# Kernel optimization log

Hardware: AMD Instinct MI355X
Metric: run time of the kernel (lower is better)

Reference implementation:

```python
import jax, jax.numpy as jnp
import numpy as np
from jax import lax

PALETTE = 256


def setup_inputs() -> dict:
    key = jax.random.key(0)
    k1, k2, k3, k4 = jax.random.split(key, 4)
    x = jax.random.normal(k1, (16, 64, 256, 256), dtype=jnp.float32)
    lookup_table = jax.random.normal(k2, (PALETTE,), dtype=jnp.float32) * 0.05
    weight_idx = jax.random.randint(k3, (64, 64, 3, 3), 0, PALETTE, dtype=jnp.int32)
    bias = jax.random.normal(k4, (64,), dtype=jnp.float32) * 0.01
    return {"x": x, "lookup_table": lookup_table, "weight_idx": weight_idx, "bias": bias}


def reference(x, lookup_table, weight_idx, bias):
    # Dequantize: palette gather produces full OIHW weight tensor.
    full_w = lookup_table[weight_idx]  # [O, I, kH, kW] float32
    # conv2d with stride=1, padding=0 (hardcoded in module), dilation=1, groups=1
    out = lax.conv_general_dilated(
        x, full_w,
        window_strides=(1, 1),
        padding='VALID',
        rhs_dilation=(1, 1),
        dimension_numbers=('NCHW', 'OIHW', 'NCHW'),
        feature_group_count=1,
    )
    return out + bias[None, :, None, None]
```

## Files before the change

kernel.cpp:

```cpp
#include <hip/hip_runtime.h>


typedef __bf16 bf16x8 __attribute__((ext_vector_type(8)));
typedef float f32x4 __attribute__((ext_vector_type(4)));
typedef float f32x2 __attribute__((ext_vector_type(2)));

union Frag {
    uint4 q;
    bf16x8 v;
};

__global__ __launch_bounds__(256) void dequant_B(
        const float* __restrict__ lut, const int* __restrict__ widx,
        uint4* __restrict__ Bws) {
    int s = blockIdx.x * 256 + threadIdx.x;
    int l = s & 63;
    int nt = (s >> 6) & 3;
    int kc = s >> 8;
    if (kc >= 18) return;
    int r = kc >> 1;
    int kh = r / 3, kw = r - kh * 3;
    int o = nt * 16 + (l & 15);
    int c0 = (kc & 1) * 32 + (l >> 4) * 8;
    Frag f;
#pragma unroll
    for (int j = 0; j < 8; ++j) {
        int c = c0 + j;
        int idx = widx[((o * 64 + c) * 3 + kh) * 3 + kw];
        f.v[j] = (__bf16)lut[idx];
    }
    Bws[s] = f.q;
}

#define A_CB 530

__global__ __launch_bounds__(256, 4) void conv_mfma(
        const float* __restrict__ x, const float* __restrict__ bias,
        const uint4* __restrict__ Bws, float* __restrict__ out) {
    __shared__ uint4 ldsA[4 * A_CB];
    unsigned* lds32 = (unsigned*)ldsA;

    int bx = blockIdx.x;
    int owt = bx & 1;
    int rem = bx >> 1;
    int ohp = rem % 127;
    int n   = rem / 127;
    int ow0 = owt * 128;
    int oh0 = ohp * 2;
    int t = threadIdx.x;

    const float* xn = x + (size_t)n * (64 * 256 * 256);

    int w = t >> 6;
    int l = t & 63;
    int l15 = l & 15, l4 = l >> 4;

    int tl_cb  = t & 3;
    int tl_rc  = t >> 2;
    int tl_rr  = tl_rc >> 1;
    int tl_col = 128 + (tl_rc & 1);
    int tl_xc  = ow0 + tl_col; if (tl_xc > 255) tl_xc = 255;

    int ohl = w >> 1;
    int ob  = (w & 1) * 2;

    f32x4 acc[8][2] = {};

    for (int h = 0; h < 2; ++h) {
        {
            const float* cbase = xn + (size_t)(((h * 4 + w) * 8 + l4 * 2)) * 65536
                                 + ow0;
#pragma unroll
            for (int ch2 = 0; ch2 < 2; ++ch2) {
                const float* pb = cbase + ch2 * 64 + l15 * 4;
                f32x4 f0[4], f1[4];
#pragma unroll
                for (int rr = 0; rr < 4; ++rr) {
                    const float* p = pb + (oh0 + rr) * 256;
                    f0[rr] = *(const f32x4*)(p);
                    f1[rr] = *(const f32x4*)(p + 65536);
                }
#pragma unroll
                for (int rr = 0; rr < 4; ++rr) {
                    int gbase = w * A_CB + rr * 132 + ch2 * 64 + l15 * 4;
#pragma unroll
                    for (int i = 0; i < 4; ++i) {
                        union { __bf16 hh[2]; unsigned u; } bp;
                        bp.hh[0] = (__bf16)f0[rr][i];
                        bp.hh[1] = (__bf16)f1[rr][i];
                        lds32[(gbase + i) * 4 + l4] = bp.u;
                    }
                }
            }
            if (t < 32) {
                const float* src = xn + (size_t)((h * 4 + tl_cb) * 8) * 65536
                                   + (oh0 + tl_rr) * 256 + tl_xc;
                Frag f;
#pragma unroll
                for (int j = 0; j < 8; ++j)
                    f.v[j] = (__bf16)src[j * 65536];
                ldsA[tl_cb * A_CB + tl_rr * 132 + tl_col] = f.q;
            }
        }
        __syncthreads();

#pragma unroll
        for (int i = 0; i < 9; ++i) {
            int kh = i / 3, kw = i - kh * 3;
            int kc = 2 * i + h;

            Frag b[2];
#pragma unroll
            for (int nt = 0; nt < 2; ++nt)
                b[nt].q = Bws[(kc * 4 + ob + nt) * 64 + l];

            Frag a[8];
#pragma unroll
            for (int mt = 0; mt < 8; ++mt)
                a[mt].q = ldsA[l4 * A_CB + (ohl + kh) * 132 + l15 + kw + mt * 16];

#pragma unroll
            for (int mt = 0; mt < 8; ++mt)
#pragma unroll
                for (int nt = 0; nt < 2; ++nt)
                    acc[mt][nt] = __builtin_amdgcn_mfma_f32_16x16x32_bf16(
                        a[mt].v, b[nt].v, acc[mt][nt], 0, 0, 0);
        }
        __syncthreads();
    }

    float* slab = (float*)ldsA + w * (16 * 130);
    int oseg = (w & 1) * 32;
    int oh = oh0 + ohl;
    float* orow = out + ((size_t)n * 64 * 254 + oh) * 254 + ow0;
    bool ok = (ow0 + l * 2 + 1) < 254;
#pragma unroll
    for (int nt = 0; nt < 2; ++nt) {
#pragma unroll
        for (int mt = 0; mt < 8; ++mt)
#pragma unroll
            for (int rg = 0; rg < 4; ++rg)
                slab[l15 * 130 + mt * 16 + l4 * 4 + rg] = acc[mt][nt][rg];
#pragma unroll
        for (int j = 0; j < 16; ++j) {
            int o = oseg + nt * 16 + j;
            float bv = bias[o];
            f32x2 v;
            v[0] = slab[j * 130 + l * 2]     + bv;
            v[1] = slab[j * 130 + l * 2 + 1] + bv;
            if (ok)
                *(f32x2*)(orow + (size_t)o * (254 * 254) + l * 2) = v;
        }
    }
}

extern "C" void kernel_launch(void* const* d_in, const int* in_sizes, int n_in,
                              void* d_out, int out_size, void* d_ws, size_t ws_size,
                              hipStream_t stream) {
    const float* x    = (const float*)d_in[0];
    const float* lut  = (const float*)d_in[1];
    const int*   widx = (const int*)d_in[2];
    const float* bias = (const float*)d_in[3];
    float* out = (float*)d_out;
    uint4* Bws = (uint4*)d_ws;

    dequant_B<<<18, 256, 0, stream>>>(lut, widx, Bws);
    conv_mfma<<<16 * 127 * 2, 256, 0, stream>>>(x, bias, (const uint4*)Bws, out);
}
```

Before: 490.9 us.

## Process full output row width per block with 512 threads to share halo

Each block now computes two full 254-wide output rows using 8 waves instead of two 128-wide halves with 4 waves. This removes the separate halo-column staging path and the redundant reloads of overlapping input columns across blocks. In exchange the block uses roughly twice the LDS, which limits how many blocks fit per CU, and the epilogue slab stride changes to 129.

```diff
diff --git a/kernel.cpp b/kernel.cpp
--- a/kernel.cpp
+++ b/kernel.cpp
@@ -32,20 +32,18 @@
     Bws[s] = f.q;
 }
 
-#define A_CB 530
+#define A_ROW 258
+#define A_CBL 1034
 
-__global__ __launch_bounds__(256, 4) void conv_mfma(
+__global__ __launch_bounds__(512, 4) void conv_mfma(
         const float* __restrict__ x, const float* __restrict__ bias,
         const uint4* __restrict__ Bws, float* __restrict__ out) {
-    __shared__ uint4 ldsA[4 * A_CB];
+    __shared__ uint4 ldsA[4136];
     unsigned* lds32 = (unsigned*)ldsA;
 
     int bx = blockIdx.x;
-    int owt = bx & 1;
-    int rem = bx >> 1;
-    int ohp = rem % 127;
-    int n   = rem / 127;
-    int ow0 = owt * 128;
+    int ohp = bx % 127;
+    int n   = bx / 127;
     int oh0 = ohp * 2;
     int t = threadIdx.x;
 
@@ -55,51 +53,39 @@
     int l = t & 63;
     int l15 = l & 15, l4 = l >> 4;
 
-    int tl_cb  = t & 3;
-    int tl_rc  = t >> 2;
-    int tl_rr  = tl_rc >> 1;
-    int tl_col = 128 + (tl_rc & 1);
-    int tl_xc  = ow0 + tl_col; if (tl_xc > 255) tl_xc = 255;
-
-    int ohl = w >> 1;
-    int ob  = (w & 1) * 2;
+    int st_cbl = w & 3;
+    int st_rp  = w >> 2;
+    int ohl = (w >> 2) & 1;
+    int owh = (w >> 1) & 1;
+    int og  = w & 1;
 
     f32x4 acc[8][2] = {};
 
     for (int h = 0; h < 2; ++h) {
         {
-            const float* cbase = xn + (size_t)(((h * 4 + w) * 8 + l4 * 2)) * 65536
-                                 + ow0;
+            const float* cb = xn
+                + (size_t)((h * 4 + st_cbl) * 8 + l4 * 2) * 65536 + l15 * 4;
 #pragma unroll
-            for (int ch2 = 0; ch2 < 2; ++ch2) {
-                const float* pb = cbase + ch2 * 64 + l15 * 4;
+            for (int rr = 0; rr < 2; ++rr) {
+                int row = st_rp * 2 + rr;
+                const float* pr = cb + (oh0 + row) * 256;
                 f32x4 f0[4], f1[4];
 #pragma unroll
-                for (int rr = 0; rr < 4; ++rr) {
-                    const float* p = pb + (oh0 + rr) * 256;
-                    f0[rr] = *(const f32x4*)(p);
-                    f1[rr] = *(const f32x4*)(p + 65536);
+                for (int cb2 = 0; cb2 < 4; ++cb2) {
+                    f0[cb2] = *(const f32x4*)(pr + cb2 * 64);
+                    f1[cb2] = *(const f32x4*)(pr + cb2 * 64 + 65536);
                 }
 #pragma unroll
-                for (int rr = 0; rr < 4; ++rr) {
-                    int gbase = w * A_CB + rr * 132 + ch2 * 64 + l15 * 4;
+                for (int cb2 = 0; cb2 < 4; ++cb2) {
+                    int gbase = st_cbl * A_CBL + row * A_ROW + cb2 * 64 + l15 * 4;
 #pragma unroll
                     for (int i = 0; i < 4; ++i) {
                         union { __bf16 hh[2]; unsigned u; } bp;
-                        bp.hh[0] = (__bf16)f0[rr][i];
-                        bp.hh[1] = (__bf16)f1[rr][i];
+                        bp.hh[0] = (__bf16)f0[cb2][i];
+                        bp.hh[1] = (__bf16)f1[cb2][i];
                         lds32[(gbase + i) * 4 + l4] = bp.u;
                     }
                 }
-            }
-            if (t < 32) {
-                const float* src = xn + (size_t)((h * 4 + tl_cb) * 8) * 65536
-                                   + (oh0 + tl_rr) * 256 + tl_xc;
-                Frag f;
-#pragma unroll
-                for (int j = 0; j < 8; ++j)
-                    f.v[j] = (__bf16)src[j * 65536];
-                ldsA[tl_cb * A_CB + tl_rr * 132 + tl_col] = f.q;
             }
         }
         __syncthreads();
@@ -112,12 +98,13 @@
             Frag b[2];
 #pragma unroll
             for (int nt = 0; nt < 2; ++nt)
-                b[nt].q = Bws[(kc * 4 + ob + nt) * 64 + l];
+                b[nt].q = Bws[(kc * 4 + og * 2 + nt) * 64 + l];
 
             Frag a[8];
 #pragma unroll
             for (int mt = 0; mt < 8; ++mt)
-                a[mt].q = ldsA[l4 * A_CB + (ohl + kh) * 132 + l15 + kw + mt * 16];
+                a[mt].q = ldsA[l4 * A_CBL + (ohl + kh) * A_ROW
+                               + owh * 128 + mt * 16 + l15 + kw];
 
 #pragma unroll
             for (int mt = 0; mt < 8; ++mt)
@@ -129,27 +116,25 @@
         __syncthreads();
     }
 
-    float* slab = (float*)ldsA + w * (16 * 130);
-    int oseg = (w & 1) * 32;
+    float* slab = (float*)ldsA + w * 2064;
     int oh = oh0 + ohl;
-    float* orow = out + ((size_t)n * 64 * 254 + oh) * 254 + ow0;
-    bool ok = (ow0 + l * 2 + 1) < 254;
 #pragma unroll
     for (int nt = 0; nt < 2; ++nt) {
 #pragma unroll
         for (int mt = 0; mt < 8; ++mt)
 #pragma unroll
             for (int rg = 0; rg < 4; ++rg)
-                slab[l15 * 130 + mt * 16 + l4 * 4 + rg] = acc[mt][nt][rg];
+                slab[l15 * 129 + mt * 16 + l4 * 4 + rg] = acc[mt][nt][rg];
 #pragma unroll
         for (int j = 0; j < 16; ++j) {
-            int o = oseg + nt * 16 + j;
+            int o = og * 32 + nt * 16 + j;
             float bv = bias[o];
             f32x2 v;
-            v[0] = slab[j * 130 + l * 2]     + bv;
-            v[1] = slab[j * 130 + l * 2 + 1] + bv;
-            if (ok)
-                *(f32x2*)(orow + (size_t)o * (254 * 254) + l * 2) = v;
+            v[0] = slab[j * 129 + 2 * l] + bv;
+            v[1] = slab[j * 129 + 2 * l + 1] + bv;
+            int col = owh * 128 + 2 * l;
+            if (col + 1 < 254)
+                *(f32x2*)(out + (((size_t)n * 64 + o) * 254 + oh) * 254 + col) = v;
         }
     }
 }
@@ -165,5 +150,5 @@
     uint4* Bws = (uint4*)d_ws;
 
     dequant_B<<<18, 256, 0, stream>>>(lut, widx, Bws);
-    conv_mfma<<<16 * 127 * 2, 256, 0, stream>>>(x, bias, (const uint4*)Bws, out);
+    conv_mfma<<<16 * 127, 512, 0, stream>>>(x, bias, (const uint4*)Bws, out);
 }
```

New measurement: 500.8 us. 2.0% more time.

## Software-pipeline global prefetch of second channel half behind first-half MFMA compute

Applied to the files above, without the earlier changes.

Restructures the two-phase conv loop so the global loads for the second half of input channels are issued before the first half's MFMA compute, and all B fragments for a phase are preloaded into registers. Barriers are replaced with a custom lgkmcnt-only wait plus s_barrier so outstanding global loads are not drained at sync points. Launch bounds drop from 4 to 2 waves-per-EU minimum to make room for the extra prefetch and B registers, trading occupancy for memory latency hiding.

```diff
diff --git a/kernel.cpp b/kernel.cpp
--- a/kernel.cpp
+++ b/kernel.cpp
@@ -9,6 +9,11 @@
     uint4 q;
     bf16x8 v;
 };
+
+#define LGKM_BARRIER() do { \
+    asm volatile("s_waitcnt lgkmcnt(0)" ::: "memory"); \
+    __builtin_amdgcn_s_barrier(); \
+    asm volatile("" ::: "memory"); } while (0)
 
 __global__ __launch_bounds__(256) void dequant_B(
         const float* __restrict__ lut, const int* __restrict__ widx,
@@ -34,7 +39,7 @@
 
 #define A_CB 530
 
-__global__ __launch_bounds__(256, 4) void conv_mfma(
+__global__ __launch_bounds__(256, 2) void conv_mfma(
         const float* __restrict__ x, const float* __restrict__ bias,
         const uint4* __restrict__ Bws, float* __restrict__ out) {
     __shared__ uint4 ldsA[4 * A_CB];
@@ -65,69 +70,97 @@
     int ob  = (w & 1) * 2;
 
     f32x4 acc[8][2] = {};
-
-    for (int h = 0; h < 2; ++h) {
-        {
-            const float* cbase = xn + (size_t)(((h * 4 + w) * 8 + l4 * 2)) * 65536
-                                 + ow0;
-#pragma unroll
-            for (int ch2 = 0; ch2 < 2; ++ch2) {
-                const float* pb = cbase + ch2 * 64 + l15 * 4;
-                f32x4 f0[4], f1[4];
-#pragma unroll
-                for (int rr = 0; rr < 4; ++rr) {
-                    const float* p = pb + (oh0 + rr) * 256;
-                    f0[rr] = *(const f32x4*)(p);
-                    f1[rr] = *(const f32x4*)(p + 65536);
-                }
-#pragma unroll
-                for (int rr = 0; rr < 4; ++rr) {
-                    int gbase = w * A_CB + rr * 132 + ch2 * 64 + l15 * 4;
-#pragma unroll
-                    for (int i = 0; i < 4; ++i) {
-                        union { __bf16 hh[2]; unsigned u; } bp;
-                        bp.hh[0] = (__bf16)f0[rr][i];
-                        bp.hh[1] = (__bf16)f1[rr][i];
-                        lds32[(gbase + i) * 4 + l4] = bp.u;
-                    }
+    uint4 breg[18];
+    f32x4 pf0[8], pf1[8];
+    float tpre[8];
+
+    auto loadB = [&](int h) {
+#pragma unroll
+        for (int i = 0; i < 9; ++i) {
+            int kc = 2 * i + h;
+            breg[i * 2 + 0] = Bws[(kc * 4 + ob + 0) * 64 + l];
+            breg[i * 2 + 1] = Bws[(kc * 4 + ob + 1) * 64 + l];
+        }
+    };
+
+    auto prefA = [&](int h) {
+        const float* cbase = xn + (size_t)((h * 4 + w) * 8 + l4 * 2) * 65536 + ow0;
+#pragma unroll
+        for (int ch2 = 0; ch2 < 2; ++ch2) {
+            const float* pb = cbase + ch2 * 64 + l15 * 4;
+#pragma unroll
+            for (int rr = 0; rr < 4; ++rr) {
+                const float* p = pb + (oh0 + rr) * 256;
+                pf0[ch2 * 4 + rr] = *(const f32x4*)(p);
+                pf1[ch2 * 4 + rr] = *(const f32x4*)(p + 65536);
+            }
+        }
+        if (t < 32) {
+            const float* src = xn + (size_t)((h * 4 + tl_cb) * 8) * 65536
+                               + (oh0 + tl_rr) * 256 + tl_xc;
+#pragma unroll
+            for (int j = 0; j < 8; ++j)
+                tpre[j] = src[j * 65536];
+        }
+    };
+
+    auto writeA = [&]() {
+#pragma unroll
+        for (int ch2 = 0; ch2 < 2; ++ch2)
+#pragma unroll
+            for (int rr = 0; rr < 4; ++rr) {
+                int gbase = w * A_CB + rr * 132 + ch2 * 64 + l15 * 4;
+#pragma unroll
+                for (int i = 0; i < 4; ++i) {
+                    union { __bf16 hh[2]; unsigned u; } bp;
+                    bp.hh[0] = (__bf16)pf0[ch2 * 4 + rr][i];
+                    bp.hh[1] = (__bf16)pf1[ch2 * 4 + rr][i];
+                    lds32[(gbase + i) * 4 + l4] = bp.u;
                 }
             }
-            if (t < 32) {
-                const float* src = xn + (size_t)((h * 4 + tl_cb) * 8) * 65536
-                                   + (oh0 + tl_rr) * 256 + tl_xc;
-                Frag f;
-#pragma unroll
-                for (int j = 0; j < 8; ++j)
-                    f.v[j] = (__bf16)src[j * 65536];
-                ldsA[tl_cb * A_CB + tl_rr * 132 + tl_col] = f.q;
-            }
-        }
-        __syncthreads();
-
+        if (t < 32) {
+            Frag f;
+#pragma unroll
+            for (int j = 0; j < 8; ++j)
+                f.v[j] = (__bf16)tpre[j];
+            ldsA[tl_cb * A_CB + tl_rr * 132 + tl_col] = f.q;
+        }
+    };
+
+    auto compute = [&]() {
 #pragma unroll
         for (int i = 0; i < 9; ++i) {
             int kh = i / 3, kw = i - kh * 3;
-            int kc = 2 * i + h;
-
-            Frag b[2];
-#pragma unroll
-            for (int nt = 0; nt < 2; ++nt)
-                b[nt].q = Bws[(kc * 4 + ob + nt) * 64 + l];
-
+            Frag b0, b1;
+            b0.q = breg[i * 2 + 0];
+            b1.q = breg[i * 2 + 1];
             Frag a[8];
 #pragma unroll
             for (int mt = 0; mt < 8; ++mt)
                 a[mt].q = ldsA[l4 * A_CB + (ohl + kh) * 132 + l15 + kw + mt * 16];
-
-#pragma unroll
-            for (int mt = 0; mt < 8; ++mt)
-#pragma unroll
-                for (int nt = 0; nt < 2; ++nt)
-                    acc[mt][nt] = __builtin_amdgcn_mfma_f32_16x16x32_bf16(
-                        a[mt].v, b[nt].v, acc[mt][nt], 0, 0, 0);
-        }
-        __syncthreads();
-    }
+#pragma unroll
+            for (int mt = 0; mt < 8; ++mt) {
+                acc[mt][0] = __builtin_amdgcn_mfma_f32_16x16x32_bf16(
+                    a[mt].v, b0.v, acc[mt][0], 0, 0, 0);
+                acc[mt][1] = __builtin_amdgcn_mfma_f32_16x16x32_bf16(
+                    a[mt].v, b1.v, acc[mt][1], 0, 0, 0);
+            }
+        }
+    };
+
+    loadB(0);
+    prefA(0);
+    writeA();
+    LGKM_BARRIER();
+    prefA(1);
+    asm volatile("" ::: "memory");
+    compute();
+    loadB(1);
+    LGKM_BARRIER();
+    writeA();
+    LGKM_BARRIER();
+    compute();
+    LGKM_BARRIER();
 
     float* slab = (float*)ldsA + w * (16 * 130);
     int oseg = (w & 1) * 32;
```

Measured after the change: 487.2 us (median of 2 runs). No clear change (-0.8%).
